# Optimization experiments

Measured on AMD Instinct MI355X. Metric: run time of the kernel, lower is better.

The kernel has to match this reference:

```python
import jax, jax.numpy as jnp
import numpy as np

FEAT_DIM = 32
RES = 256
N_GAUSS = 500000
KSIZE = 5
SIGMA = 1.0


def setup_inputs() -> dict:
    key = jax.random.key(0)
    k0, k1, k2, k3, k4 = jax.random.split(key, 5)
    plane_xy = jax.random.normal(k0, (1, FEAT_DIM, RES, RES), jnp.float32)
    plane_xz = jax.random.normal(k1, (1, FEAT_DIM, RES, RES), jnp.float32)
    plane_yz = jax.random.normal(k2, (1, FEAT_DIM, RES, RES), jnp.float32)
    ln_weight = jnp.ones((FEAT_DIM, RES, RES), jnp.float32)
    ln_bias = jnp.zeros((FEAT_DIM, RES, RES), jnp.float32)
    gaussian_features = jax.random.normal(k3, (N_GAUSS, 3 * FEAT_DIM), jnp.float32)
    gaussian_xyz = jax.random.uniform(k4, (N_GAUSS, 3), jnp.float32, -1.0, 1.0)
    return {"plane_xy": plane_xy, "plane_xz": plane_xz, "plane_yz": plane_yz,
            "ln_weight": ln_weight, "ln_bias": ln_bias,
            "gaussian_features": gaussian_features, "gaussian_xyz": gaussian_xyz}


def _gaussian_blur(x):
    # depthwise 5x5 gaussian blur, groups = channels
    c = x.shape[1]
    k = jnp.arange(-(KSIZE // 2), KSIZE // 2 + 1, dtype=jnp.float32)
    k = jnp.exp(-0.5 * (k / SIGMA) ** 2)
    k = k / k.sum()
    k2d = k[:, None] * k[None, :]                       # [5,5]
    kern = jnp.broadcast_to(k2d, (c, 1, KSIZE, KSIZE))  # OIHW, grouped
    return jax.lax.conv_general_dilated(
        x, kern, window_strides=(1, 1), padding="SAME",
        feature_group_count=c,
        dimension_numbers=("NCHW", "OIHW", "NCHW"))


def _update_plane(plane, idx, feats, ln_w, ln_b):
    # plane [1,C,H,W]; idx [N,2] float pixel coords (x,y); feats [N,C]
    _, C, H, W = plane.shape
    px, py = idx[:, 0], idx[:, 1]
    px0 = jnp.clip(jnp.floor(px).astype(jnp.int32), 0, W - 1)
    px1 = jnp.clip(jnp.floor(px).astype(jnp.int32) + 1, 0, W - 1)
    py0 = jnp.clip(jnp.floor(py).astype(jnp.int32), 0, H - 1)
    py1 = jnp.clip(jnp.floor(py).astype(jnp.int32) + 1, 0, H - 1)
    wx0 = jnp.clip(px1.astype(px.dtype) - px, 0.0, 1.0)
    wx1 = jnp.clip(px - px0.astype(px.dtype), 0.0, 1.0)
    wy0 = jnp.clip(py1.astype(py.dtype) - py, 0.0, 1.0)
    wy1 = jnp.clip(py - py0.astype(py.dtype), 0.0, 1.0)
    weights = jnp.stack([wx0 * wy0, wx0 * wy1, wx1 * wy0, wx1 * wy1], axis=-1)  # [N,4]
    iy = jnp.stack([py0, py1, py0, py1], axis=-1)  # [N,4]
    ix = jnp.stack([px0, px0, px1, px1], axis=-1)  # [N,4]
    lin = (iy * W + ix).reshape(-1)                # [N*4]
    wf = (feats[:, None, :] * weights[:, :, None]).reshape(-1, C)  # [N*4, C]
    acc = jnp.zeros((H * W, C), plane.dtype).at[lin].add(wf)       # scatter-add
    counts = jnp.zeros((H * W,), plane.dtype).at[lin].add(1.0)
    flat = plane.reshape(C, H * W)
    # straight-through: value = scattered features, grad flows identity to plane
    new = flat + jax.lax.stop_gradient(-flat) + acc.T
    new = new / (counts[None, :] + 1e-6)
    new = new.reshape(1, C, H, W)
    # LayerNorm over (C,H,W)
    mu = jnp.mean(new, axis=(1, 2, 3), keepdims=True)
    var = jnp.var(new, axis=(1, 2, 3), keepdims=True)
    new = (new - mu) / jnp.sqrt(var + 1e-5) * ln_w[None] + ln_b[None]
    new = _gaussian_blur(new)
    return new + plane


def reference(plane_xy, plane_xz, plane_yz, ln_weight, ln_bias,
              gaussian_features, gaussian_xyz):
    res = plane_xy.shape[-1]
    xyz01 = (gaussian_xyz + 1.0) / 2.0
    x = jnp.clip(xyz01[..., 0], 0.0, 0.999) * (res - 1)
    y = jnp.clip(xyz01[..., 1], 0.0, 0.999) * (res - 1)
    z = jnp.clip(xyz01[..., 2], 0.0, 0.999) * (res - 1)
    feats = gaussian_features.reshape(gaussian_xyz.shape[0], 3, -1)
    new_xy = _update_plane(plane_xy, jnp.stack([x, y], -1), feats[:, 0, :], ln_weight, ln_bias)
    new_xz = _update_plane(plane_xz, jnp.stack([x, z], -1), feats[:, 1, :], ln_weight, ln_bias)
    new_yz = _update_plane(plane_yz, jnp.stack([y, z], -1), feats[:, 2, :], ln_weight, ln_bias)
    return (new_xy, new_xz, new_yz)
```

## Files before the change

### kernel.cpp

```cpp
#include <hip/hip_runtime.h>
#include <hip/hip_bf16.h>

#define N_GAUSS 500000
#define NGP (N_GAUSS * 3)
#define FEAT 32
#define RES 256
#define HW (RES * RES)
#define PLANE_ELEMS (FEAT * HW)
#define NBINS (3 * HW)

typedef __hip_bfloat16 bf16;

__device__ __forceinline__ bool input_is_bf16(const void* lnw) {
  return ((const unsigned int*)lnw)[0] == 0x3F803F80u;
}

template <bool BF16>
__device__ __forceinline__ float ldin(const void* p, size_t i) {
  if constexpr (BF16)
    return __bfloat162float(((const bf16*)p)[i]);
  else
    return ((const float*)p)[i];
}

template <bool BF16>
__device__ __forceinline__ void stout(void* p, size_t i, float v) {
  if constexpr (BF16)
    ((bf16*)p)[i] = __float2bfloat16(v);
  else
    ((float*)p)[i] = v;
}

template <bool BF16>
__device__ __forceinline__ void gpos(const void* xyz, int g, int p, float& px,
                                     float& py) {
  int dx = (p == 2) ? 1 : 0;
  int dy = (p == 0) ? 1 : 2;
  float vx = ldin<BF16>(xyz, 3 * g + dx);
  float vy = ldin<BF16>(xyz, 3 * g + dy);
  px = fminf(fmaxf((vx + 1.0f) * 0.5f, 0.0f), 0.999f) * (float)(RES - 1);
  py = fminf(fmaxf((vy + 1.0f) * 0.5f, 0.0f), 0.999f) * (float)(RES - 1);
}

template <bool BF16>
__device__ __forceinline__ void count_impl(const void* xyz,
                                           int* __restrict__ bincnt) {
  int t = blockIdx.x * 256 + threadIdx.x;
  if (t >= NGP) return;
  int g = t / 3;
  int p = t - g * 3;
  float px, py;
  gpos<BF16>(xyz, g, p, px, py);
  atomicAdd(&bincnt[(p << 16) + ((int)py << 8) + (int)px], 1);
}

__global__ __launch_bounds__(256) void count_kernel(const void* __restrict__ xyz,
                                                    const void* __restrict__ lnw,
                                                    int* __restrict__ bincnt) {
  if (input_is_bf16(lnw))
    count_impl<true>(xyz, bincnt);
  else
    count_impl<false>(xyz, bincnt);
}

__global__ __launch_bounds__(256) void scan1_kernel(const int* __restrict__ bincnt,
                                                    int* __restrict__ off,
                                                    int* __restrict__ bsum) {
  int tid = threadIdx.x;
  int4 v = ((const int4*)bincnt)[blockIdx.x * 256 + tid];
  int s = v.x + v.y + v.z + v.w;
  __shared__ int ls[256];
  ls[tid] = s;
  __syncthreads();
  for (int o = 1; o < 256; o <<= 1) {
    int t = 0;
    if (tid >= o) t = ls[tid - o];
    __syncthreads();
    ls[tid] += t;
    __syncthreads();
  }
  int excl = ls[tid] - s;
  int base = blockIdx.x * 1024 + tid * 4;
  off[base + 0] = excl;
  off[base + 1] = excl + v.x;
  off[base + 2] = excl + v.x + v.y;
  off[base + 3] = excl + v.x + v.y + v.z;
  if (tid == 255) bsum[blockIdx.x] = ls[255];
}

__global__ __launch_bounds__(256) void scan2_kernel(const int* __restrict__ bsum,
                                                    int* __restrict__ bbase) {
  int tid = threadIdx.x;
  int v = (tid < 192) ? bsum[tid] : 0;
  __shared__ int ls[256];
  ls[tid] = v;
  __syncthreads();
  for (int o = 1; o < 256; o <<= 1) {
    int t = 0;
    if (tid >= o) t = ls[tid - o];
    __syncthreads();
    ls[tid] += t;
    __syncthreads();
  }
  if (tid < 192) bbase[tid] = ls[tid] - v;
}

__global__ __launch_bounds__(256) void scan3_kernel(int* __restrict__ off,
                                                    const int* __restrict__ bbase) {
  int i = blockIdx.x * 256 + threadIdx.x;
  off[i] += bbase[i >> 10];
}

template <bool BF16>
__device__ __forceinline__ void scatter_impl(const void* xyz,
                                             int* __restrict__ off,
                                             int* __restrict__ entries) {
  int t = blockIdx.x * 256 + threadIdx.x;
  if (t >= NGP) return;
  int g = t / 3;
  int p = t - g * 3;
  float px, py;
  gpos<BF16>(xyz, g, p, px, py);
  int slot = atomicAdd(&off[(p << 16) + ((int)py << 8) + (int)px], 1);
  entries[slot * 3 + 0] = __float_as_int(px);
  entries[slot * 3 + 1] = __float_as_int(py);
  entries[slot * 3 + 2] = t << 5;
}

__global__ __launch_bounds__(256) void scatter_kernel(
    const void* __restrict__ xyz, const void* __restrict__ lnw,
    int* __restrict__ off, int* __restrict__ entries) {
  if (input_is_bf16(lnw))
    scatter_impl<true>(xyz, off, entries);
  else
    scatter_impl<false>(xyz, off, entries);
}

template <bool BF16>
__device__ __forceinline__ void gather_impl(const int* __restrict__ off,
                                            const int* __restrict__ bincnt,
                                            const int* __restrict__ entries,
                                            const void* __restrict__ feats,
                                            float* __restrict__ nb,
                                            float* tile) {
  int wid = threadIdx.x >> 6;
  int lane = threadIdx.x & 63;
  int c = lane & 31;
  int sub = lane >> 5;
  int pid4 = (blockIdx.x * 4 + wid) * 4;
  int p = pid4 >> 16;
  int pix = pid4 & 65535;
  int y = pix >> 8;
  int x0 = pix & 255;
  float fyq = (float)y;
  float fx0f = (float)x0;

  int bxlo = max(x0 - 1, 0);
  int rbA = (p << 16) + ((y - 1) << 8);
  int rbB = (p << 16) + (y << 8);
  int sA = 0, eA = 0;
  if (y > 0) {
    int bA0 = rbA + bxlo;
    sA = off[bA0] - bincnt[bA0];
    eA = off[rbA + x0 + 3];
  }
  int bB0 = rbB + bxlo;
  int sB = off[bB0] - bincnt[bB0];
  int eB = off[rbB + x0 + 3];

  int s0 = 0, s1 = 0, s2 = 0, s3 = 0, s4 = 0;
  {
    int col;
    col = x0 - 1;
    if (col >= 0) {
      s0 = bincnt[rbB + col];
      if (y > 0) s0 += bincnt[rbA + col];
    }
    col = x0;
    s1 = bincnt[rbB + col];
    if (y > 0) s1 += bincnt[rbA + col];
    col = x0 + 1;
    s2 = bincnt[rbB + col];
    if (y > 0) s2 += bincnt[rbA + col];
    col = x0 + 2;
    s3 = bincnt[rbB + col];
    if (y > 0) s3 += bincnt[rbA + col];
    col = x0 + 3;
    s4 = bincnt[rbB + col];
    if (y > 0) s4 += bincnt[rbA + col];
  }
  int cnt0 = s0 + s1, cnt1 = s1 + s2, cnt2 = s2 + s3, cnt3 = s3 + s4;

  float a0 = 0.0f, a1 = 0.0f, a2 = 0.0f, a3 = 0.0f;
#pragma unroll 1
  for (int rr = 0; rr < 2; ++rr) {
    int start = rr ? sB : sA;
    int end = rr ? eB : eA;
#pragma unroll 1
    for (int base = start; base < end; base += 20) {
      int n = end - base;
      n = n > 20 ? 20 : n;
      int d = 0;
      if (lane < n * 3) d = entries[base * 3 + lane];
#pragma unroll 1
      for (int k = 0; k < n; k += 2) {
        int idx = k + sub;
        bool act = idx < n;
        int j3 = (act ? idx : 0) * 3;
        float epx = __int_as_float(__shfl(d, j3));
        float epy = __int_as_float(__shfl(d, j3 + 1));
        int fb = __shfl(d, j3 + 2);
        float wy = 1.0f - fabsf(epy - fyq);
        if (!act) wy = 0.0f;
        float f = ldin<BF16>(feats, (size_t)fb + c);
        float wf = wy * f;
        a0 += fmaxf(1.0f - fabsf(epx - fx0f), 0.0f) * wf;
        a1 += fmaxf(1.0f - fabsf(epx - (fx0f + 1.0f)), 0.0f) * wf;
        a2 += fmaxf(1.0f - fabsf(epx - (fx0f + 2.0f)), 0.0f) * wf;
        a3 += fmaxf(1.0f - fabsf(epx - (fx0f + 3.0f)), 0.0f) * wf;
      }
    }
  }
  a0 += __shfl_xor(a0, 32);
  a1 += __shfl_xor(a1, 32);
  a2 += __shfl_xor(a2, 32);
  a3 += __shfl_xor(a3, 32);
  if (sub == 0) {
    int lb = (wid << 2);
    tile[c * 17 + lb + 0] = a0 / ((float)cnt0 + 1e-6f);
    tile[c * 17 + lb + 1] = a1 / ((float)cnt1 + 1e-6f);
    tile[c * 17 + lb + 2] = a2 / ((float)cnt2 + 1e-6f);
    tile[c * 17 + lb + 3] = a3 / ((float)cnt3 + 1e-6f);
  }
  __syncthreads();
  int c2 = threadIdx.x >> 4;
  int lp = threadIdx.x & 15;
  int pix0 = (blockIdx.x << 4) & 65535;
  size_t b = ((size_t)p << 21) + pix0 + lp;
  nb[b + ((size_t)c2 << 16)] = tile[c2 * 17 + lp];
  nb[b + ((size_t)(c2 + 16) << 16)] = tile[(c2 + 16) * 17 + lp];
}

__global__ __launch_bounds__(256) void gather_kernel(
    const int* __restrict__ off, const int* __restrict__ bincnt,
    const int* __restrict__ entries, const void* __restrict__ feats,
    const void* __restrict__ lnw, float* __restrict__ nb) {
  __shared__ float tile[32 * 17];
  if (input_is_bf16(lnw))
    gather_impl<true>(off, bincnt, entries, feats, nb, tile);
  else
    gather_impl<false>(off, bincnt, entries, feats, nb, tile);
}

__global__ __launch_bounds__(256) void stats_kernel(const float* __restrict__ nb,
                                                    double* __restrict__ stats) {
  int b = blockIdx.x;
  int p = b >> 8;
  int blk = b & 255;
  const float4* nb4 = (const float4*)(nb + ((size_t)p << 21));
  int tid = threadIdx.x;
  float s = 0.0f, s2 = 0.0f;
#pragma unroll
  for (int k = 0; k < 8; ++k) {
    float4 v = nb4[blk * 2048 + k * 256 + tid];
    s += (v.x + v.y) + (v.z + v.w);
    s2 += (v.x * v.x + v.y * v.y) + (v.z * v.z + v.w * v.w);
  }
  __shared__ float ls[256];
  __shared__ float ls2[256];
  ls[tid] = s;
  ls2[tid] = s2;
  __syncthreads();
  for (int o = 128; o > 0; o >>= 1) {
    if (tid < o) {
      ls[tid] += ls[tid + o];
      ls2[tid] += ls2[tid + o];
    }
    __syncthreads();
  }
  if (tid == 0) {
    unsafeAtomicAdd(&stats[2 * p + 0], (double)ls[0]);
    unsafeAtomicAdd(&stats[2 * p + 1], (double)ls2[0]);
  }
}

template <bool BF16>
__device__ __forceinline__ void blur_impl(const float* __restrict__ nb,
                                          const double* __restrict__ stats,
                                          const void* __restrict__ lnw,
                                          const void* __restrict__ lnb,
                                          const void* __restrict__ pl,
                                          void* __restrict__ out,
                                          float (*sm)[36]) {
  int p = blockIdx.z >> 5;
  int c = blockIdx.z & 31;
  const float* np = nb + ((size_t)p << 21) + ((size_t)c << 16);

  double mu_d = stats[2 * p] * (1.0 / PLANE_ELEMS);
  double var_d = stats[2 * p + 1] * (1.0 / PLANE_ELEMS) - mu_d * mu_d;
  float mu = (float)mu_d;
  float inv = rsqrtf((float)var_d + 1e-5f);

  int tx = threadIdx.x, ty = threadIdx.y;
  int w0 = blockIdx.x * 32, h0 = blockIdx.y * 8;
  int lid = ty * 32 + tx;
  for (int li = lid; li < 12 * 36; li += 256) {
    int r = li / 36;
    int q = li - r * 36;
    int hh = h0 - 2 + r;
    int ww = w0 - 2 + q;
    float v = 0.0f;
    if ((unsigned)hh < 256u && (unsigned)ww < 256u) {
      int pix = (hh << 8) + ww;
      float a = np[pix];
      size_t gi = ((size_t)c << 16) + pix;
      v = (a - mu) * inv * ldin<BF16>(lnw, gi) + ldin<BF16>(lnb, gi);
    }
    sm[r][q] = v;
  }
  __syncthreads();

  const float K[5] = {0.054488685f, 0.24420134f, 0.40261996f, 0.24420134f,
                      0.054488685f};
  float a = 0.0f;
#pragma unroll
  for (int i = 0; i < 5; i++) {
    float rs = 0.0f;
#pragma unroll
    for (int j = 0; j < 5; j++) rs += K[j] * sm[ty + i][tx + j];
    a += K[i] * rs;
  }
  size_t idx = ((size_t)c << 16) + ((h0 + ty) << 8) + w0 + tx;
  float res = a + ldin<BF16>(pl, idx);
  stout<BF16>(out, ((size_t)p << 21) + idx, res);
}

__global__ __launch_bounds__(256) void blur_kernel(
    const float* __restrict__ nb, const double* __restrict__ stats,
    const void* __restrict__ lnw, const void* __restrict__ lnb,
    const void* __restrict__ p0, const void* __restrict__ p1,
    const void* __restrict__ p2, void* __restrict__ out) {
  __shared__ float sm[12][36];
  int p = blockIdx.z >> 5;
  const void* pl = (p == 0) ? p0 : ((p == 1) ? p1 : p2);
  if (input_is_bf16(lnw))
    blur_impl<true>(nb, stats, lnw, lnb, pl, out, sm);
  else
    blur_impl<false>(nb, stats, lnw, lnb, pl, out, sm);
}

extern "C" void kernel_launch(void* const* d_in, const int* in_sizes, int n_in,
                              void* d_out, int out_size, void* d_ws,
                              size_t ws_size, hipStream_t stream) {
  const void* plane_xy = d_in[0];
  const void* plane_xz = d_in[1];
  const void* plane_yz = d_in[2];
  const void* lnw = d_in[3];
  const void* lnb = d_in[4];
  const void* feats = d_in[5];
  const void* xyz = d_in[6];

  char* ws = (char*)d_ws;
  int* bincnt = (int*)ws;
  double* stats = (double*)(ws + 786432);
  int* off = (int*)(ws + 786480);
  int* bsum = (int*)(ws + 1572912);
  int* bbase = (int*)(ws + 1573680);
  int* entries = (int*)(ws + 1574448);
  float* nb = (float*)(ws + 19574448);

  hipMemsetAsync(d_ws, 0, 786480, stream);

  int gp_blocks = (NGP + 255) / 256;
  count_kernel<<<gp_blocks, 256, 0, stream>>>(xyz, lnw, bincnt);
  scan1_kernel<<<192, 256, 0, stream>>>(bincnt, off, bsum);
  scan2_kernel<<<1, 256, 0, stream>>>(bsum, bbase);
  scan3_kernel<<<NBINS / 256, 256, 0, stream>>>(off, bbase);
  scatter_kernel<<<gp_blocks, 256, 0, stream>>>(xyz, lnw, off, entries);
  gather_kernel<<<NBINS / 16, 256, 0, stream>>>(off, bincnt, entries, feats,
                                                lnw, nb);
  stats_kernel<<<768, 256, 0, stream>>>(nb, stats);
  blur_kernel<<<dim3(8, 32, 96), dim3(32, 8), 0, stream>>>(
      nb, stats, lnw, lnb, plane_xy, plane_xz, plane_yz, d_out);
}
```

Baseline: 681.3 us.

## Fuse scan passes, precompute gather weights per lane, vectorize blur tile loads

Three separate changes. The second and third scan kernels become one: every block redoes the small 192-entry block-sum scan in shared memory, which removes a launch and a dependent kernel boundary at the cost of redundant work in each block. In the gather loop, each lane computes its entry's bilinear x/y weights once per 20-entry chunk, and the inner loop fetches them with shuffles instead of recomputing the weights for every pair. The blur tile load reads two adjacent pixels at a time with float2 and bf16x2 loads to halve the load instruction count.

```diff
diff --git a/kernel.cpp b/kernel.cpp
--- a/kernel.cpp
+++ b/kernel.cpp
@@ -21,6 +21,17 @@
     return __bfloat162float(((const bf16*)p)[i]);
   else
     return ((const float*)p)[i];
+}
+
+template <bool BF16>
+__device__ __forceinline__ float2 ldin2(const void* p, size_t i) {
+  if constexpr (BF16) {
+    unsigned u = *(const unsigned*)((const bf16*)p + i);
+    return make_float2(__uint_as_float(u << 16),
+                       __uint_as_float(u & 0xFFFF0000u));
+  } else {
+    return *(const float2*)((const float*)p + i);
+  }
 }
 
 template <bool BF16>
@@ -88,11 +99,12 @@
   if (tid == 255) bsum[blockIdx.x] = ls[255];
 }
 
-__global__ __launch_bounds__(256) void scan2_kernel(const int* __restrict__ bsum,
-                                                    int* __restrict__ bbase) {
+__global__ __launch_bounds__(256) void scan23_kernel(int* __restrict__ off,
+                                                     const int* __restrict__ bsum) {
+  __shared__ int ls[256];
+  __shared__ int ex[192];
   int tid = threadIdx.x;
   int v = (tid < 192) ? bsum[tid] : 0;
-  __shared__ int ls[256];
   ls[tid] = v;
   __syncthreads();
   for (int o = 1; o < 256; o <<= 1) {
@@ -102,13 +114,10 @@
     ls[tid] += t;
     __syncthreads();
   }
-  if (tid < 192) bbase[tid] = ls[tid] - v;
-}
-
-__global__ __launch_bounds__(256) void scan3_kernel(int* __restrict__ off,
-                                                    const int* __restrict__ bbase) {
-  int i = blockIdx.x * 256 + threadIdx.x;
-  off[i] += bbase[i >> 10];
+  if (tid < 192) ex[tid] = ls[tid] - v;
+  __syncthreads();
+  int i = blockIdx.x * 256 + tid;
+  off[i] += ex[blockIdx.x >> 2];
 }
 
 template <bool BF16>
@@ -202,22 +211,27 @@
       n = n > 20 ? 20 : n;
       int d = 0;
       if (lane < n * 3) d = entries[base * 3 + lane];
+      int l = lane < 20 ? lane : 19;
+      float epx = __int_as_float(__shfl(d, 3 * l + 0));
+      float epy = __int_as_float(__shfl(d, 3 * l + 1));
+      int fbp = __shfl(d, 3 * l + 2);
+      float wy = 1.0f - fabsf(epy - fyq);
+      float u = epx - fx0f;
+      float w0p = fmaxf(1.0f - fabsf(u), 0.0f) * wy;
+      float w1p = fmaxf(1.0f - fabsf(u - 1.0f), 0.0f) * wy;
+      float w2p = fmaxf(1.0f - fabsf(u - 2.0f), 0.0f) * wy;
+      float w3p = fmaxf(1.0f - fabsf(u - 3.0f), 0.0f) * wy;
 #pragma unroll 1
       for (int k = 0; k < n; k += 2) {
         int idx = k + sub;
-        bool act = idx < n;
-        int j3 = (act ? idx : 0) * 3;
-        float epx = __int_as_float(__shfl(d, j3));
-        float epy = __int_as_float(__shfl(d, j3 + 1));
-        int fb = __shfl(d, j3 + 2);
-        float wy = 1.0f - fabsf(epy - fyq);
-        if (!act) wy = 0.0f;
+        int is = idx < n ? idx : 0;
+        int fb = __shfl(fbp, is);
         float f = ldin<BF16>(feats, (size_t)fb + c);
-        float wf = wy * f;
-        a0 += fmaxf(1.0f - fabsf(epx - fx0f), 0.0f) * wf;
-        a1 += fmaxf(1.0f - fabsf(epx - (fx0f + 1.0f)), 0.0f) * wf;
-        a2 += fmaxf(1.0f - fabsf(epx - (fx0f + 2.0f)), 0.0f) * wf;
-        a3 += fmaxf(1.0f - fabsf(epx - (fx0f + 3.0f)), 0.0f) * wf;
+        if (idx >= n) f = 0.0f;
+        a0 = fmaf(__shfl(w0p, is), f, a0);
+        a1 = fmaf(__shfl(w1p, is), f, a1);
+        a2 = fmaf(__shfl(w2p, is), f, a2);
+        a3 = fmaf(__shfl(w3p, is), f, a3);
       }
     }
   }
@@ -304,19 +318,23 @@
   int tx = threadIdx.x, ty = threadIdx.y;
   int w0 = blockIdx.x * 32, h0 = blockIdx.y * 8;
   int lid = ty * 32 + tx;
-  for (int li = lid; li < 12 * 36; li += 256) {
-    int r = li / 36;
-    int q = li - r * 36;
+  for (int li = lid; li < 12 * 18; li += 256) {
+    int r = li / 18;
+    int m = li - r * 18;
     int hh = h0 - 2 + r;
-    int ww = w0 - 2 + q;
-    float v = 0.0f;
+    int ww = w0 - 2 + (m << 1);
+    float v0 = 0.0f, v1 = 0.0f;
     if ((unsigned)hh < 256u && (unsigned)ww < 256u) {
       int pix = (hh << 8) + ww;
-      float a = np[pix];
+      float2 av = *(const float2*)(np + pix);
       size_t gi = ((size_t)c << 16) + pix;
-      v = (a - mu) * inv * ldin<BF16>(lnw, gi) + ldin<BF16>(lnb, gi);
+      float2 lw = ldin2<BF16>(lnw, gi);
+      float2 lb = ldin2<BF16>(lnb, gi);
+      v0 = (av.x - mu) * inv * lw.x + lb.x;
+      v1 = (av.y - mu) * inv * lw.y + lb.y;
     }
-    sm[r][q] = v;
+    sm[r][(m << 1) + 0] = v0;
+    sm[r][(m << 1) + 1] = v1;
   }
   __syncthreads();
 
@@ -365,7 +383,6 @@
   double* stats = (double*)(ws + 786432);
   int* off = (int*)(ws + 786480);
   int* bsum = (int*)(ws + 1572912);
-  int* bbase = (int*)(ws + 1573680);
   int* entries = (int*)(ws + 1574448);
   float* nb = (float*)(ws + 19574448);
 
@@ -374,8 +391,7 @@
   int gp_blocks = (NGP + 255) / 256;
   count_kernel<<<gp_blocks, 256, 0, stream>>>(xyz, lnw, bincnt);
   scan1_kernel<<<192, 256, 0, stream>>>(bincnt, off, bsum);
-  scan2_kernel<<<1, 256, 0, stream>>>(bsum, bbase);
-  scan3_kernel<<<NBINS / 256, 256, 0, stream>>>(off, bbase);
+  scan23_kernel<<<NBINS / 256, 256, 0, stream>>>(off, bsum);
   scatter_kernel<<<gp_blocks, 256, 0, stream>>>(xyz, lnw, off, entries);
   gather_kernel<<<NBINS / 16, 256, 0, stream>>>(off, bincnt, entries, feats,
                                                 lnw, nb);
```

Measured after the change: 685.9 us. About the same (+0.7%).
